# Optimization experiments

Measured on AMD Instinct MI355X. Metric: run time of the kernel, lower is better.

Reference implementation:

```python
import jax, jax.numpy as jnp
import numpy as np

B, S, D, H = 2, 2048, 1024, 16
HD = D // H  # head_dim = 64

def setup_inputs() -> dict:
    key = jax.random.key(0)
    ks = jax.random.split(key, 5)
    scale = 1.0 / np.sqrt(D)
    x = jax.random.normal(ks[0], (B, S, D), dtype=jnp.float32)
    Wq = jax.random.normal(ks[1], (D, D), dtype=jnp.float32) * scale
    Wk = jax.random.normal(ks[2], (D, D), dtype=jnp.float32) * scale
    Wv = jax.random.normal(ks[3], (D, D), dtype=jnp.float32) * scale
    Wf = jax.random.normal(ks[4], (D, D), dtype=jnp.float32) * scale
    z = jnp.zeros((D,), dtype=jnp.float32)
    return {"x": x, "Wq": Wq, "bq": z, "Wk": Wk, "bk": z, "Wv": Wv, "bv": z, "Wf": Wf, "bf": z}

def reference(x, Wq, bq, Wk, bk, Wv, bv, Wf, bf):
    # Linear layers follow torch convention: y = x @ W.T + b
    def split_heads(t):  # [B,S,D] -> [B,H,S,HD]
        return t.reshape(B, S, H, HD).transpose(0, 2, 1, 3)
    q = split_heads(x @ Wq.T + bq)
    k = split_heads(x @ Wk.T + bk)
    v = split_heads(x @ Wv.T + bv)
    scores = jnp.einsum('bhqd,bhkd->bhqk', q, k) / jnp.sqrt(jnp.float32(HD))
    causal = jnp.tril(jnp.ones((S, S), dtype=bool))  # [S,S]
    scores = jnp.where(causal[None, None], scores, -jnp.inf)
    attn = jax.nn.softmax(scores, axis=-1)
    out = jnp.einsum('bhqk,bhkd->bhqd', attn, v)
    out = out.transpose(0, 2, 1, 3).reshape(B, S, D)
    return out @ Wf.T + bf
```

## Files before the change

kernel.cpp:

```cpp
#include <hip/hip_runtime.h>
#include <stdint.h>

#define B_  2
#define S_  2048
#define D_  1024
#define H_  16
#define HD_ 64
#define M_  (B_*S_)

typedef __bf16 bf16x8 __attribute__((ext_vector_type(8)));
typedef float  f32x4  __attribute__((ext_vector_type(4)));

typedef const __attribute__((address_space(1))) void* gas_ptr;
typedef __attribute__((address_space(3))) void* las_ptr;

__device__ __forceinline__ uint16_t f32_to_bf16(float f) {
  uint32_t u = __float_as_uint(f);
  u += 0x7FFFu + ((u >> 16) & 1u);
  return (uint16_t)(u >> 16);
}

__device__ __forceinline__ void g2l16(const uint16_t* g, uint16_t* l) {
  __builtin_amdgcn_global_load_lds((gas_ptr)g, (las_ptr)l, 16, 0, 0);
}

__global__ void cast_all(const float* __restrict__ x,
                         const float* __restrict__ wq, const float* __restrict__ wk,
                         const float* __restrict__ wv, const float* __restrict__ wf,
                         uint16_t* __restrict__ xb,
                         uint16_t* __restrict__ wqb, uint16_t* __restrict__ wkb,
                         uint16_t* __restrict__ wvb, uint16_t* __restrict__ wfb) {
  const int X4 = M_ * D_ / 4;
  const int W4 = D_ * D_ / 4;
  int i = blockIdx.x * 256 + threadIdx.x;
  const float* src; uint16_t* dst; int off;
  if (i < X4) { src = x; dst = xb; off = i; }
  else {
    int j = i - X4;
    int w = j >> 18;
    off = j & (W4 - 1);
    src = (w == 0) ? wq : (w == 1) ? wk : (w == 2) ? wv : wf;
    dst = (w == 0) ? wqb : (w == 1) ? wkb : (w == 2) ? wvb : wfb;
  }
  float4 v = ((const float4*)src)[off];
  ushort4 o;
  o.x = f32_to_bf16(v.x); o.y = f32_to_bf16(v.y);
  o.z = f32_to_bf16(v.z); o.w = f32_to_bf16(v.w);
  ((ushort4*)dst)[off] = o;
}

__device__ __forceinline__ void gemm_tile_1024(
    const uint16_t* __restrict__ A, const uint16_t* __restrict__ B,
    int am0, int bn0, uint16_t* As, uint16_t* Bs, f32x4 (&acc)[4][4])
{
  const int tid  = threadIdx.x;
  const int wave = tid >> 6;
  const int lane = tid & 63;
  const int quad = lane >> 4;
  const int l16  = lane & 15;
  const int wm = (wave >> 1) * 64;
  const int wn = (wave & 1) * 64;

  #pragma unroll
  for (int i = 0; i < 4; ++i)
    #pragma unroll
    for (int j = 0; j < 4; ++j)
      #pragma unroll
      for (int e = 0; e < 4; ++e)
        acc[i][j][e] = 0.f;

  const int seg0 = wave * 64 + lane;
  const int seg1 = seg0 + 256;
  uint16_t* lA0 = As + (size_t)(wave * 64) * 8;
  uint16_t* lA1 = As + (size_t)(256 + wave * 64) * 8;
  uint16_t* lB0 = Bs + (size_t)(wave * 64) * 8;
  uint16_t* lB1 = Bs + (size_t)(256 + wave * 64) * 8;
  const uint16_t* gA0 = A + (size_t)(am0 + (seg0 >> 2)) * D_ + (seg0 & 3) * 8;
  const uint16_t* gA1 = A + (size_t)(am0 + (seg1 >> 2)) * D_ + (seg1 & 3) * 8;
  const uint16_t* gB0 = B + (size_t)(bn0 + (seg0 >> 2)) * D_ + (seg0 & 3) * 8;
  const uint16_t* gB1 = B + (size_t)(bn0 + (seg1 >> 2)) * D_ + (seg1 & 3) * 8;

  for (int k0 = 0; k0 < D_; k0 += 32) {
    g2l16(gA0 + k0, lA0);
    g2l16(gA1 + k0, lA1);
    g2l16(gB0 + k0, lB0);
    g2l16(gB1 + k0, lB1);
    __syncthreads();
    bf16x8 af[4], bfr[4];
    #pragma unroll
    for (int mt = 0; mt < 4; ++mt)
      af[mt] = *(const bf16x8*)(As + (wm + mt * 16 + l16) * 32 + quad * 8);
    #pragma unroll
    for (int nt = 0; nt < 4; ++nt)
      bfr[nt] = *(const bf16x8*)(Bs + (wn + nt * 16 + l16) * 32 + quad * 8);
    #pragma unroll
    for (int mt = 0; mt < 4; ++mt)
      #pragma unroll
      for (int nt = 0; nt < 4; ++nt)
        acc[mt][nt] = __builtin_amdgcn_mfma_f32_16x16x32_bf16(
            af[mt], bfr[nt], acc[mt][nt], 0, 0, 0);
    __syncthreads();
  }
}

__global__ __launch_bounds__(256)
void qkv_gemm(const uint16_t* __restrict__ xb,
              const uint16_t* __restrict__ wqb, const uint16_t* __restrict__ wkb,
              const uint16_t* __restrict__ wvb,
              const float* __restrict__ bqv, const float* __restrict__ bkv,
              const float* __restrict__ bvv,
              uint16_t* __restrict__ qout, uint16_t* __restrict__ kout,
              uint16_t* __restrict__ vtout)
{
  __shared__ __align__(16) uint16_t As[128 * 32];
  __shared__ __align__(16) uint16_t Bs[128 * 32];
  const int wsel = blockIdx.y >> 3;
  const int lane = threadIdx.x & 63, wave = threadIdx.x >> 6;
  const int quad = lane >> 4, l16 = lane & 15;
  const int wm = (wave >> 1) * 64, wn = (wave & 1) * 64;

  const uint16_t *Ap, *Bp;
  int m0e, n0e;
  if (wsel < 2) {
    Ap = xb; Bp = (wsel == 0) ? wqb : wkb;
    m0e = blockIdx.x * 128; n0e = (blockIdx.y & 7) * 128;
  } else {
    Ap = wvb; Bp = xb;
    m0e = (blockIdx.y & 7) * 128; n0e = blockIdx.x * 128;
  }
  f32x4 acc[4][4];
  gemm_tile_1024(Ap, Bp, m0e, n0e, As, Bs, acc);

  if (wsel < 2) {
    const float* bias = (wsel == 0) ? bqv : bkv;
    uint16_t* outp = (wsel == 0) ? qout : kout;
    const float scl = (wsel == 0) ? 0.18033688f : 1.0f;
    #pragma unroll
    for (int nt = 0; nt < 4; ++nt) {
      const int n = n0e + wn + nt * 16 + l16;
      const int h = n >> 6, hd = n & 63;
      const float bia = bias[n];
      #pragma unroll
      for (int mt = 0; mt < 4; ++mt) {
        #pragma unroll
        for (int r = 0; r < 4; ++r) {
          const int m = m0e + wm + mt * 16 + quad * 4 + r;
          const int bb = m >> 11, s = m & (S_ - 1);
          outp[(((size_t)(bb * H_ + h)) * S_ + s) * HD_ + hd] =
              f32_to_bf16((acc[mt][nt][r] + bia) * scl);
        }
      }
    }
  } else {
    #pragma unroll
    for (int mt = 0; mt < 4; ++mt) {
      #pragma unroll
      for (int r = 0; r < 4; ++r) {
        const int m = m0e + wm + mt * 16 + quad * 4 + r;
        const int h = m >> 6, hd = m & 63;
        const float bia = bvv[m];
        #pragma unroll
        for (int nt = 0; nt < 4; ++nt) {
          const int n = n0e + wn + nt * 16 + l16;
          const int bb = n >> 11, s = n & (S_ - 1);
          vtout[(((size_t)(bb * H_ + h)) * HD_ + hd) * S_ + s] =
              f32_to_bf16(acc[mt][nt][r] + bia);
        }
      }
    }
  }
}

__global__ __launch_bounds__(256)
void flash_attn(const uint16_t* __restrict__ qb, const uint16_t* __restrict__ kb,
                const uint16_t* __restrict__ vtb, uint16_t* __restrict__ ao)
{
  __shared__ __align__(16) uint16_t ks[2][64 * 32];
  __shared__ __align__(16) uint16_t vs[2][64 * 32];
  __shared__ __align__(16) uint16_t p_lds[4][16][72];

  const int bh = blockIdx.x;
  const int qt = (int)(gridDim.y - 1u - blockIdx.y);
  const int wave = threadIdx.x >> 6, lane = threadIdx.x & 63;
  const int quad = lane >> 4, l16 = lane & 15;
  const int q0 = qt * 64;

  const uint16_t* Q  = qb  + (size_t)bh * S_ * HD_;
  const uint16_t* Kp = kb  + (size_t)bh * S_ * HD_;
  const uint16_t* Vt = vtb + (size_t)bh * HD_ * S_;

  const int qrow = q0 + wave * 16;
  bf16x8 aq0 = *(const bf16x8*)(Q + (size_t)(qrow + l16) * HD_ + quad * 8);
  bf16x8 aq1 = *(const bf16x8*)(Q + (size_t)(qrow + l16) * HD_ + 32 + quad * 8);

  const uint16_t* sb[4]; uint16_t* sdst[4]; int sstep[4];
  #pragma unroll
  for (int j = 0; j < 4; ++j) {
    const int g = wave * 4 + j;
    if (g < 8) {
      const int c = (g >> 2) & 1, rb = g & 3;
      sdst[j] = &ks[c][rb * 512];
      sb[j] = Kp + (size_t)(rb * 16 + (lane >> 2)) * HD_ + c * 32 + (lane & 3) * 8;
      sstep[j] = 64 * HD_;
    } else {
      const int gg = g - 8, c = (gg >> 2) & 1, rb = gg & 3;
      sdst[j] = &vs[c][rb * 512];
      sb[j] = Vt + (size_t)(rb * 16 + (lane >> 2)) * S_ + c * 32 + (lane & 3) * 8;
      sstep[j] = 64;
    }
  }

  float lpart[4];
  f32x4 o[4];
  #pragma unroll
  for (int r = 0; r < 4; ++r) lpart[r] = 0.f;
  #pragma unroll
  for (int t = 0; t < 4; ++t)
    #pragma unroll
    for (int e = 0; e < 4; ++e) o[t][e] = 0.f;

  const int rowid = qrow + quad * 4;

  for (int kt = 0; kt <= qt; ++kt) {
    const int kbase = kt * 64;
    const bool diag = (kt == qt);

    #pragma unroll
    for (int j = 0; j < 4; ++j) {
      g2l16(sb[j], sdst[j]);
      sb[j] += sstep[j];
    }
    __syncthreads();

    bf16x8 kf0[4], kf1[4];
    #pragma unroll
    for (int nt = 0; nt < 4; ++nt) {
      kf0[nt] = *(const bf16x8*)(&ks[0][(nt * 16 + l16) * 32 + quad * 8]);
      kf1[nt] = *(const bf16x8*)(&ks[1][(nt * 16 + l16) * 32 + quad * 8]);
    }
    f32x4 sacc[4];
    #pragma unroll
    for (int nt = 0; nt < 4; ++nt) {
      #pragma unroll
      for (int e = 0; e < 4; ++e) sacc[nt][e] = 0.f;
      sacc[nt] = __builtin_amdgcn_mfma_f32_16x16x32_bf16(aq0, kf0[nt], sacc[nt], 0, 0, 0);
      sacc[nt] = __builtin_amdgcn_mfma_f32_16x16x32_bf16(aq1, kf1[nt], sacc[nt], 0, 0, 0);
    }

    bf16x8 vf0[4], vf1[4];
    #pragma unroll
    for (int t = 0; t < 4; ++t) {
      vf0[t] = *(const bf16x8*)(&vs[0][(t * 16 + l16) * 32 + quad * 8]);
      vf1[t] = *(const bf16x8*)(&vs[1][(t * 16 + l16) * 32 + quad * 8]);
    }

    #pragma unroll
    for (int nt = 0; nt < 4; ++nt) {
      const int kkc = kbase + nt * 16 + l16;
      #pragma unroll
      for (int r = 0; r < 4; ++r) {
        float p = __builtin_amdgcn_exp2f(sacc[nt][r]);
        if (diag && (kkc > rowid + r)) p = 0.f;
        lpart[r] += p;
        p_lds[wave][quad * 4 + r][nt * 16 + l16] = f32_to_bf16(p);
      }
    }

    bf16x8 ap0 = *(const bf16x8*)(&p_lds[wave][l16][quad * 8]);
    bf16x8 ap1 = *(const bf16x8*)(&p_lds[wave][l16][32 + quad * 8]);
    #pragma unroll
    for (int t = 0; t < 4; ++t) {
      o[t] = __builtin_amdgcn_mfma_f32_16x16x32_bf16(ap0, vf0[t], o[t], 0, 0, 0);
      o[t] = __builtin_amdgcn_mfma_f32_16x16x32_bf16(ap1, vf1[t], o[t], 0, 0, 0);
    }
    __syncthreads();
  }

  #pragma unroll
  for (int r = 0; r < 4; ++r) {
    lpart[r] += __shfl_xor(lpart[r], 1, 64);
    lpart[r] += __shfl_xor(lpart[r], 2, 64);
    lpart[r] += __shfl_xor(lpart[r], 4, 64);
    lpart[r] += __shfl_xor(lpart[r], 8, 64);
  }
  const int bb = bh >> 4, h = bh & 15;
  #pragma unroll
  for (int t = 0; t < 4; ++t) {
    #pragma unroll
    for (int r = 0; r < 4; ++r) {
      const float ov = o[t][r] / lpart[r];
      ao[((size_t)(bb * S_ + rowid + r)) * D_ + h * HD_ + t * 16 + l16] =
          f32_to_bf16(ov);
    }
  }
}

__global__ __launch_bounds__(256)
void out_gemm(const uint16_t* __restrict__ ab, const uint16_t* __restrict__ wfb,
              const float* __restrict__ bfv, float* __restrict__ out)
{
  __shared__ __align__(16) uint16_t As[64 * 32];
  __shared__ __align__(16) uint16_t Bs[128 * 32];
  const int m0 = blockIdx.x * 64;
  const int n0 = blockIdx.y * 128;
  const int lane = threadIdx.x & 63, wave = threadIdx.x >> 6;
  const int quad = lane >> 4, l16 = lane & 15;
  const int wm = (wave >> 1) * 32, wn = (wave & 1) * 64;

  f32x4 acc[2][4];
  #pragma unroll
  for (int i = 0; i < 2; ++i)
    #pragma unroll
    for (int j = 0; j < 4; ++j)
      #pragma unroll
      for (int e = 0; e < 4; ++e)
        acc[i][j][e] = 0.f;

  const int segA = wave * 64 + lane;
  const int segB0 = segA, segB1 = segA + 256;
  uint16_t* lA  = As + (size_t)(wave * 64) * 8;
  uint16_t* lB0 = Bs + (size_t)(wave * 64) * 8;
  uint16_t* lB1 = Bs + (size_t)(256 + wave * 64) * 8;
  const uint16_t* gA  = ab  + (size_t)(m0 + (segA  >> 2)) * D_ + (segA  & 3) * 8;
  const uint16_t* gB0 = wfb + (size_t)(n0 + (segB0 >> 2)) * D_ + (segB0 & 3) * 8;
  const uint16_t* gB1 = wfb + (size_t)(n0 + (segB1 >> 2)) * D_ + (segB1 & 3) * 8;

  for (int k0 = 0; k0 < D_; k0 += 32) {
    g2l16(gA  + k0, lA);
    g2l16(gB0 + k0, lB0);
    g2l16(gB1 + k0, lB1);
    __syncthreads();
    bf16x8 af[2], bfr[4];
    #pragma unroll
    for (int mt = 0; mt < 2; ++mt)
      af[mt] = *(const bf16x8*)(As + (wm + mt * 16 + l16) * 32 + quad * 8);
    #pragma unroll
    for (int nt = 0; nt < 4; ++nt)
      bfr[nt] = *(const bf16x8*)(Bs + (wn + nt * 16 + l16) * 32 + quad * 8);
    #pragma unroll
    for (int mt = 0; mt < 2; ++mt)
      #pragma unroll
      for (int nt = 0; nt < 4; ++nt)
        acc[mt][nt] = __builtin_amdgcn_mfma_f32_16x16x32_bf16(
            af[mt], bfr[nt], acc[mt][nt], 0, 0, 0);
    __syncthreads();
  }

  #pragma unroll
  for (int nt = 0; nt < 4; ++nt) {
    const int n = n0 + wn + nt * 16 + l16;
    const float bia = bfv[n];
    #pragma unroll
    for (int mt = 0; mt < 2; ++mt) {
      #pragma unroll
      for (int r = 0; r < 4; ++r) {
        const int m = m0 + wm + mt * 16 + quad * 4 + r;
        out[(size_t)m * D_ + n] = acc[mt][nt][r] + bia;
      }
    }
  }
}

extern "C" void kernel_launch(void* const* d_in, const int* in_sizes, int n_in,
                              void* d_out, int out_size, void* d_ws, size_t ws_size,
                              hipStream_t stream) {
  (void)in_sizes; (void)n_in; (void)out_size; (void)ws_size;
  const float* x  = (const float*)d_in[0];
  const float* Wq = (const float*)d_in[1];
  const float* bq = (const float*)d_in[2];
  const float* Wk = (const float*)d_in[3];
  const float* bk = (const float*)d_in[4];
  const float* Wv = (const float*)d_in[5];
  const float* bv = (const float*)d_in[6];
  const float* Wf = (const float*)d_in[7];
  const float* bf = (const float*)d_in[8];
  float* out = (float*)d_out;

  uint16_t* ws = (uint16_t*)d_ws;
  uint16_t* xb   = ws;
  uint16_t* wqb  = xb  + (size_t)M_ * D_;
  uint16_t* wkb  = wqb + (size_t)D_ * D_;
  uint16_t* wvb  = wkb + (size_t)D_ * D_;
  uint16_t* wfb  = wvb + (size_t)D_ * D_;
  uint16_t* qbuf = wfb + (size_t)D_ * D_;
  uint16_t* kbuf = qbuf + (size_t)M_ * D_;
  uint16_t* vtb  = kbuf + (size_t)M_ * D_;
  uint16_t* aob  = vtb  + (size_t)M_ * D_;

  const int CAST_BLOCKS = (M_ * D_ / 4 + 4 * (D_ * D_ / 4)) / 256;
  cast_all<<<CAST_BLOCKS, 256, 0, stream>>>(x, Wq, Wk, Wv, Wf,
                                            xb, wqb, wkb, wvb, wfb);

  qkv_gemm<<<dim3(32, 24), 256, 0, stream>>>(xb, wqb, wkb, wvb, bq, bk, bv,
                                             qbuf, kbuf, vtb);
  flash_attn<<<dim3(32, 32), 256, 0, stream>>>(qbuf, kbuf, vtb, aob);
  out_gemm<<<dim3(64, 8), 256, 0, stream>>>(aob, wfb, bf, out);
}
```

Before: 198.3 us.

## Swizzle LDS tile layout and shrink QKV GEMM tile to 64x128

Applies an XOR swizzle to the 16-byte chunks staged into LDS via global_load_lds (permuting source addresses) and matches it in the fragment reads for the GEMMs and the flash-attention K/V tiles, to reduce LDS bank conflicts. The QKV GEMM tile shrinks from 128x128 to 64x128, doubling the grid to give more blocks and better occupancy, and out_gemm now reuses the shared tile routine. Smaller tiles mean more redundant global loads per FLOP.

```diff
diff --git a/kernel.cpp b/kernel.cpp
--- a/kernel.cpp
+++ b/kernel.cpp
@@ -22,6 +22,10 @@
 
 __device__ __forceinline__ void g2l16(const uint16_t* g, uint16_t* l) {
   __builtin_amdgcn_global_load_lds((gas_ptr)g, (las_ptr)l, 16, 0, 0);
+}
+
+__device__ __forceinline__ int swz_src(int s) {
+  return (s >> 2) * D_ + (((s & 3) ^ ((s >> 3) & 3)) * 8);
 }
 
 __global__ void cast_all(const float* __restrict__ x,
@@ -49,52 +53,50 @@
   ((ushort4*)dst)[off] = o;
 }
 
-__device__ __forceinline__ void gemm_tile_1024(
+__device__ __forceinline__ void gemm_tile_64x128(
     const uint16_t* __restrict__ A, const uint16_t* __restrict__ B,
-    int am0, int bn0, uint16_t* As, uint16_t* Bs, f32x4 (&acc)[4][4])
+    int am0, int bn0, uint16_t* As, uint16_t* Bs, f32x4 (&acc)[2][4])
 {
   const int tid  = threadIdx.x;
   const int wave = tid >> 6;
   const int lane = tid & 63;
   const int quad = lane >> 4;
   const int l16  = lane & 15;
-  const int wm = (wave >> 1) * 64;
+  const int wm = (wave >> 1) * 32;
   const int wn = (wave & 1) * 64;
-
-  #pragma unroll
-  for (int i = 0; i < 4; ++i)
+  const int sw = quad ^ ((l16 >> 1) & 3);
+
+  #pragma unroll
+  for (int i = 0; i < 2; ++i)
     #pragma unroll
     for (int j = 0; j < 4; ++j)
       #pragma unroll
       for (int e = 0; e < 4; ++e)
         acc[i][j][e] = 0.f;
 
-  const int seg0 = wave * 64 + lane;
-  const int seg1 = seg0 + 256;
-  uint16_t* lA0 = As + (size_t)(wave * 64) * 8;
-  uint16_t* lA1 = As + (size_t)(256 + wave * 64) * 8;
+  const int sA  = wave * 64 + lane;
+  const int sB1 = sA + 256;
+  uint16_t* lA  = As + (size_t)(wave * 64) * 8;
   uint16_t* lB0 = Bs + (size_t)(wave * 64) * 8;
   uint16_t* lB1 = Bs + (size_t)(256 + wave * 64) * 8;
-  const uint16_t* gA0 = A + (size_t)(am0 + (seg0 >> 2)) * D_ + (seg0 & 3) * 8;
-  const uint16_t* gA1 = A + (size_t)(am0 + (seg1 >> 2)) * D_ + (seg1 & 3) * 8;
-  const uint16_t* gB0 = B + (size_t)(bn0 + (seg0 >> 2)) * D_ + (seg0 & 3) * 8;
-  const uint16_t* gB1 = B + (size_t)(bn0 + (seg1 >> 2)) * D_ + (seg1 & 3) * 8;
+  const uint16_t* gA  = A + (size_t)am0 * D_ + swz_src(sA);
+  const uint16_t* gB0 = B + (size_t)bn0 * D_ + swz_src(sA);
+  const uint16_t* gB1 = B + (size_t)bn0 * D_ + swz_src(sB1);
 
   for (int k0 = 0; k0 < D_; k0 += 32) {
-    g2l16(gA0 + k0, lA0);
-    g2l16(gA1 + k0, lA1);
+    g2l16(gA  + k0, lA);
     g2l16(gB0 + k0, lB0);
     g2l16(gB1 + k0, lB1);
     __syncthreads();
-    bf16x8 af[4], bfr[4];
-    #pragma unroll
-    for (int mt = 0; mt < 4; ++mt)
-      af[mt] = *(const bf16x8*)(As + (wm + mt * 16 + l16) * 32 + quad * 8);
+    bf16x8 af[2], bfr[4];
+    #pragma unroll
+    for (int mt = 0; mt < 2; ++mt)
+      af[mt] = *(const bf16x8*)(As + ((wm + mt * 16 + l16) * 4 + sw) * 8);
     #pragma unroll
     for (int nt = 0; nt < 4; ++nt)
-      bfr[nt] = *(const bf16x8*)(Bs + (wn + nt * 16 + l16) * 32 + quad * 8);
-    #pragma unroll
-    for (int mt = 0; mt < 4; ++mt)
+      bfr[nt] = *(const bf16x8*)(Bs + ((wn + nt * 16 + l16) * 4 + sw) * 8);
+    #pragma unroll
+    for (int mt = 0; mt < 2; ++mt)
       #pragma unroll
       for (int nt = 0; nt < 4; ++nt)
         acc[mt][nt] = __builtin_amdgcn_mfma_f32_16x16x32_bf16(
@@ -112,24 +114,25 @@
               uint16_t* __restrict__ qout, uint16_t* __restrict__ kout,
               uint16_t* __restrict__ vtout)
 {
-  __shared__ __align__(16) uint16_t As[128 * 32];
+  __shared__ __align__(16) uint16_t As[64 * 32];
   __shared__ __align__(16) uint16_t Bs[128 * 32];
   const int wsel = blockIdx.y >> 3;
   const int lane = threadIdx.x & 63, wave = threadIdx.x >> 6;
   const int quad = lane >> 4, l16 = lane & 15;
-  const int wm = (wave >> 1) * 64, wn = (wave & 1) * 64;
+  const int wm = (wave >> 1) * 32, wn = (wave & 1) * 64;
 
   const uint16_t *Ap, *Bp;
   int m0e, n0e;
   if (wsel < 2) {
     Ap = xb; Bp = (wsel == 0) ? wqb : wkb;
-    m0e = blockIdx.x * 128; n0e = (blockIdx.y & 7) * 128;
+    m0e = blockIdx.x * 64; n0e = (blockIdx.y & 7) * 128;
   } else {
+    const int vi = (blockIdx.y & 7) * 64 + blockIdx.x;
     Ap = wvb; Bp = xb;
-    m0e = (blockIdx.y & 7) * 128; n0e = blockIdx.x * 128;
-  }
-  f32x4 acc[4][4];
-  gemm_tile_1024(Ap, Bp, m0e, n0e, As, Bs, acc);
+    m0e = (vi & 15) * 64; n0e = (vi >> 4) * 128;
+  }
+  f32x4 acc[2][4];
+  gemm_tile_64x128(Ap, Bp, m0e, n0e, As, Bs, acc);
 
   if (wsel < 2) {
     const float* bias = (wsel == 0) ? bqv : bkv;
@@ -141,7 +144,7 @@
       const int h = n >> 6, hd = n & 63;
       const float bia = bias[n];
       #pragma unroll
-      for (int mt = 0; mt < 4; ++mt) {
+      for (int mt = 0; mt < 2; ++mt) {
         #pragma unroll
         for (int r = 0; r < 4; ++r) {
           const int m = m0e + wm + mt * 16 + quad * 4 + r;
@@ -153,7 +156,7 @@
     }
   } else {
     #pragma unroll
-    for (int mt = 0; mt < 4; ++mt) {
+    for (int mt = 0; mt < 2; ++mt) {
       #pragma unroll
       for (int r = 0; r < 4; ++r) {
         const int m = m0e + wm + mt * 16 + quad * 4 + r;
@@ -183,6 +186,7 @@
   const int qt = (int)(gridDim.y - 1u - blockIdx.y);
   const int wave = threadIdx.x >> 6, lane = threadIdx.x & 63;
   const int quad = lane >> 4, l16 = lane & 15;
+  const int sw = quad ^ ((l16 >> 1) & 3);
   const int q0 = qt * 64;
 
   const uint16_t* Q  = qb  + (size_t)bh * S_ * HD_;
@@ -193,6 +197,8 @@
   bf16x8 aq0 = *(const bf16x8*)(Q + (size_t)(qrow + l16) * HD_ + quad * 8);
   bf16x8 aq1 = *(const bf16x8*)(Q + (size_t)(qrow + l16) * HD_ + 32 + quad * 8);
 
+  const int srow = lane >> 2;
+  const int schk = (lane & 3) ^ ((lane >> 3) & 3);
   const uint16_t* sb[4]; uint16_t* sdst[4]; int sstep[4];
   #pragma unroll
   for (int j = 0; j < 4; ++j) {
@@ -200,12 +206,12 @@
     if (g < 8) {
       const int c = (g >> 2) & 1, rb = g & 3;
       sdst[j] = &ks[c][rb * 512];
-      sb[j] = Kp + (size_t)(rb * 16 + (lane >> 2)) * HD_ + c * 32 + (lane & 3) * 8;
+      sb[j] = Kp + (size_t)(rb * 16 + srow) * HD_ + c * 32 + schk * 8;
       sstep[j] = 64 * HD_;
     } else {
       const int gg = g - 8, c = (gg >> 2) & 1, rb = gg & 3;
       sdst[j] = &vs[c][rb * 512];
-      sb[j] = Vt + (size_t)(rb * 16 + (lane >> 2)) * S_ + c * 32 + (lane & 3) * 8;
+      sb[j] = Vt + (size_t)(rb * 16 + srow) * S_ + c * 32 + schk * 8;
       sstep[j] = 64;
     }
   }
@@ -235,8 +241,8 @@
     bf16x8 kf0[4], kf1[4];
     #pragma unroll
     for (int nt = 0; nt < 4; ++nt) {
-      kf0[nt] = *(const bf16x8*)(&ks[0][(nt * 16 + l16) * 32 + quad * 8]);
-      kf1[nt] = *(const bf16x8*)(&ks[1][(nt * 16 + l16) * 32 + quad * 8]);
+      kf0[nt] = *(const bf16x8*)(&ks[0][((nt * 16 + l16) * 4 + sw) * 8]);
+      kf1[nt] = *(const bf16x8*)(&ks[1][((nt * 16 + l16) * 4 + sw) * 8]);
     }
     f32x4 sacc[4];
     #pragma unroll
@@ -250,8 +256,8 @@
     bf16x8 vf0[4], vf1[4];
     #pragma unroll
     for (int t = 0; t < 4; ++t) {
-      vf0[t] = *(const bf16x8*)(&vs[0][(t * 16 + l16) * 32 + quad * 8]);
-      vf1[t] = *(const bf16x8*)(&vs[1][(t * 16 + l16) * 32 + quad * 8]);
+      vf0[t] = *(const bf16x8*)(&vs[0][((t * 16 + l16) * 4 + sw) * 8]);
+      vf1[t] = *(const bf16x8*)(&vs[1][((t * 16 + l16) * 4 + sw) * 8]);
     }
 
     #pragma unroll
@@ -303,49 +309,11 @@
   __shared__ __align__(16) uint16_t Bs[128 * 32];
   const int m0 = blockIdx.x * 64;
   const int n0 = blockIdx.y * 128;
+  f32x4 acc[2][4];
+  gemm_tile_64x128(ab, wfb, m0, n0, As, Bs, acc);
   const int lane = threadIdx.x & 63, wave = threadIdx.x >> 6;
   const int quad = lane >> 4, l16 = lane & 15;
   const int wm = (wave >> 1) * 32, wn = (wave & 1) * 64;
-
-  f32x4 acc[2][4];
-  #pragma unroll
-  for (int i = 0; i < 2; ++i)
-    #pragma unroll
-    for (int j = 0; j < 4; ++j)
-      #pragma unroll
-      for (int e = 0; e < 4; ++e)
-        acc[i][j][e] = 0.f;
-
-  const int segA = wave * 64 + lane;
-  const int segB0 = segA, segB1 = segA + 256;
-  uint16_t* lA  = As + (size_t)(wave * 64) * 8;
-  uint16_t* lB0 = Bs + (size_t)(wave * 64) * 8;
-  uint16_t* lB1 = Bs + (size_t)(256 + wave * 64) * 8;
-  const uint16_t* gA  = ab  + (size_t)(m0 + (segA  >> 2)) * D_ + (segA  & 3) * 8;
-  const uint16_t* gB0 = wfb + (size_t)(n0 + (segB0 >> 2)) * D_ + (segB0 & 3) * 8;
-  const uint16_t* gB1 = wfb + (size_t)(n0 + (segB1 >> 2)) * D_ + (segB1 & 3) * 8;
-
-  for (int k0 = 0; k0 < D_; k0 += 32) {
-    g2l16(gA  + k0, lA);
-    g2l16(gB0 + k0, lB0);
-    g2l16(gB1 + k0, lB1);
-    __syncthreads();
-    bf16x8 af[2], bfr[4];
-    #pragma unroll
-    for (int mt = 0; mt < 2; ++mt)
-      af[mt] = *(const bf16x8*)(As + (wm + mt * 16 + l16) * 32 + quad * 8);
-    #pragma unroll
-    for (int nt = 0; nt < 4; ++nt)
-      bfr[nt] = *(const bf16x8*)(Bs + (wn + nt * 16 + l16) * 32 + quad * 8);
-    #pragma unroll
-    for (int mt = 0; mt < 2; ++mt)
-      #pragma unroll
-      for (int nt = 0; nt < 4; ++nt)
-        acc[mt][nt] = __builtin_amdgcn_mfma_f32_16x16x32_bf16(
-            af[mt], bfr[nt], acc[mt][nt], 0, 0, 0);
-    __syncthreads();
-  }
-
   #pragma unroll
   for (int nt = 0; nt < 4; ++nt) {
     const int n = n0 + wn + nt * 16 + l16;
@@ -391,7 +359,7 @@
   cast_all<<<CAST_BLOCKS, 256, 0, stream>>>(x, Wq, Wk, Wv, Wf,
                                             xb, wqb, wkb, wvb, wfb);
 
-  qkv_gemm<<<dim3(32, 24), 256, 0, stream>>>(xb, wqb, wkb, wvb, bq, bk, bv,
+  qkv_gemm<<<dim3(64, 24), 256, 0, stream>>>(xb, wqb, wkb, wvb, bq, bk, bv,
                                              qbuf, kbuf, vtb);
   flash_attn<<<dim3(32, 32), 256, 0, stream>>>(qbuf, kbuf, vtb, aob);
   out_gemm<<<dim3(64, 8), 256, 0, stream>>>(aob, wfb, bf, out);
```

Result: faster. 194.1 us (-2.2%).

## XOR-swizzle LDS tiles to avoid bank conflicts and reorder GEMM grid

Applied to the files above, without the earlier changes.

Applies an XOR swizzle to the 16-byte chunk index when loading A/B tiles and K/V tiles into LDS: global source addresses are permuted so the direct global-to-LDS writes land swizzled, and the MFMA fragment reads use the matching swizzle. The aim is to remove LDS bank conflicts on the row-strided bf16x8 reads in all three GEMM and attention kernels. It also transposes the GEMM launch grids so consecutive blocks share the same activation rows and walk across weight tiles, which is meant to improve L2 reuse. The extra index arithmetic is small, and correctness depends on the load permutation and read swizzle matching exactly.

```diff
diff --git a/kernel.cpp b/kernel.cpp
--- a/kernel.cpp
+++ b/kernel.cpp
@@ -22,6 +22,10 @@
 
 __device__ __forceinline__ void g2l16(const uint16_t* g, uint16_t* l) {
   __builtin_amdgcn_global_load_lds((gas_ptr)g, (las_ptr)l, 16, 0, 0);
+}
+
+__device__ __forceinline__ int swz_src(int s) {
+  return (s >> 2) * D_ + (((s & 3) ^ ((s >> 3) & 3)) * 8);
 }
 
 __global__ void cast_all(const float* __restrict__ x,
@@ -49,7 +53,7 @@
   ((ushort4*)dst)[off] = o;
 }
 
-__device__ __forceinline__ void gemm_tile_1024(
+__device__ __forceinline__ void gemm_tile_128_swz(
     const uint16_t* __restrict__ A, const uint16_t* __restrict__ B,
     int am0, int bn0, uint16_t* As, uint16_t* Bs, f32x4 (&acc)[4][4])
 {
@@ -60,6 +64,7 @@
   const int l16  = lane & 15;
   const int wm = (wave >> 1) * 64;
   const int wn = (wave & 1) * 64;
+  const int sw = quad ^ ((l16 >> 1) & 3);
 
   #pragma unroll
   for (int i = 0; i < 4; ++i)
@@ -69,16 +74,16 @@
       for (int e = 0; e < 4; ++e)
         acc[i][j][e] = 0.f;
 
-  const int seg0 = wave * 64 + lane;
-  const int seg1 = seg0 + 256;
+  const int s0 = wave * 64 + lane;
+  const int s1 = s0 + 256;
   uint16_t* lA0 = As + (size_t)(wave * 64) * 8;
   uint16_t* lA1 = As + (size_t)(256 + wave * 64) * 8;
   uint16_t* lB0 = Bs + (size_t)(wave * 64) * 8;
   uint16_t* lB1 = Bs + (size_t)(256 + wave * 64) * 8;
-  const uint16_t* gA0 = A + (size_t)(am0 + (seg0 >> 2)) * D_ + (seg0 & 3) * 8;
-  const uint16_t* gA1 = A + (size_t)(am0 + (seg1 >> 2)) * D_ + (seg1 & 3) * 8;
-  const uint16_t* gB0 = B + (size_t)(bn0 + (seg0 >> 2)) * D_ + (seg0 & 3) * 8;
-  const uint16_t* gB1 = B + (size_t)(bn0 + (seg1 >> 2)) * D_ + (seg1 & 3) * 8;
+  const uint16_t* gA0 = A + (size_t)am0 * D_ + swz_src(s0);
+  const uint16_t* gA1 = A + (size_t)am0 * D_ + swz_src(s1);
+  const uint16_t* gB0 = B + (size_t)bn0 * D_ + swz_src(s0);
+  const uint16_t* gB1 = B + (size_t)bn0 * D_ + swz_src(s1);
 
   for (int k0 = 0; k0 < D_; k0 += 32) {
     g2l16(gA0 + k0, lA0);
@@ -89,10 +94,10 @@
     bf16x8 af[4], bfr[4];
     #pragma unroll
     for (int mt = 0; mt < 4; ++mt)
-      af[mt] = *(const bf16x8*)(As + (wm + mt * 16 + l16) * 32 + quad * 8);
+      af[mt] = *(const bf16x8*)(As + ((wm + mt * 16 + l16) * 4 + sw) * 8);
     #pragma unroll
     for (int nt = 0; nt < 4; ++nt)
-      bfr[nt] = *(const bf16x8*)(Bs + (wn + nt * 16 + l16) * 32 + quad * 8);
+      bfr[nt] = *(const bf16x8*)(Bs + ((wn + nt * 16 + l16) * 4 + sw) * 8);
     #pragma unroll
     for (int mt = 0; mt < 4; ++mt)
       #pragma unroll
@@ -114,7 +119,9 @@
 {
   __shared__ __align__(16) uint16_t As[128 * 32];
   __shared__ __align__(16) uint16_t Bs[128 * 32];
-  const int wsel = blockIdx.y >> 3;
+  const int wsel = blockIdx.x >> 3;
+  const int nsel = blockIdx.x & 7;
+  const int mtile = blockIdx.y;
   const int lane = threadIdx.x & 63, wave = threadIdx.x >> 6;
   const int quad = lane >> 4, l16 = lane & 15;
   const int wm = (wave >> 1) * 64, wn = (wave & 1) * 64;
@@ -123,13 +130,13 @@
   int m0e, n0e;
   if (wsel < 2) {
     Ap = xb; Bp = (wsel == 0) ? wqb : wkb;
-    m0e = blockIdx.x * 128; n0e = (blockIdx.y & 7) * 128;
+    m0e = mtile * 128; n0e = nsel * 128;
   } else {
     Ap = wvb; Bp = xb;
-    m0e = (blockIdx.y & 7) * 128; n0e = blockIdx.x * 128;
+    m0e = nsel * 128; n0e = mtile * 128;
   }
   f32x4 acc[4][4];
-  gemm_tile_1024(Ap, Bp, m0e, n0e, As, Bs, acc);
+  gemm_tile_128_swz(Ap, Bp, m0e, n0e, As, Bs, acc);
 
   if (wsel < 2) {
     const float* bias = (wsel == 0) ? bqv : bkv;
@@ -183,6 +190,7 @@
   const int qt = (int)(gridDim.y - 1u - blockIdx.y);
   const int wave = threadIdx.x >> 6, lane = threadIdx.x & 63;
   const int quad = lane >> 4, l16 = lane & 15;
+  const int sw = quad ^ ((l16 >> 1) & 3);
   const int q0 = qt * 64;
 
   const uint16_t* Q  = qb  + (size_t)bh * S_ * HD_;
@@ -193,6 +201,8 @@
   bf16x8 aq0 = *(const bf16x8*)(Q + (size_t)(qrow + l16) * HD_ + quad * 8);
   bf16x8 aq1 = *(const bf16x8*)(Q + (size_t)(qrow + l16) * HD_ + 32 + quad * 8);
 
+  const int srow = lane >> 2;
+  const int schk = (lane & 3) ^ ((lane >> 3) & 3);
   const uint16_t* sb[4]; uint16_t* sdst[4]; int sstep[4];
   #pragma unroll
   for (int j = 0; j < 4; ++j) {
@@ -200,12 +210,12 @@
     if (g < 8) {
       const int c = (g >> 2) & 1, rb = g & 3;
       sdst[j] = &ks[c][rb * 512];
-      sb[j] = Kp + (size_t)(rb * 16 + (lane >> 2)) * HD_ + c * 32 + (lane & 3) * 8;
+      sb[j] = Kp + (size_t)(rb * 16 + srow) * HD_ + c * 32 + schk * 8;
       sstep[j] = 64 * HD_;
     } else {
       const int gg = g - 8, c = (gg >> 2) & 1, rb = gg & 3;
       sdst[j] = &vs[c][rb * 512];
-      sb[j] = Vt + (size_t)(rb * 16 + (lane >> 2)) * S_ + c * 32 + (lane & 3) * 8;
+      sb[j] = Vt + (size_t)(rb * 16 + srow) * S_ + c * 32 + schk * 8;
       sstep[j] = 64;
     }
   }
@@ -235,8 +245,8 @@
     bf16x8 kf0[4], kf1[4];
     #pragma unroll
     for (int nt = 0; nt < 4; ++nt) {
-      kf0[nt] = *(const bf16x8*)(&ks[0][(nt * 16 + l16) * 32 + quad * 8]);
-      kf1[nt] = *(const bf16x8*)(&ks[1][(nt * 16 + l16) * 32 + quad * 8]);
+      kf0[nt] = *(const bf16x8*)(&ks[0][((nt * 16 + l16) * 4 + sw) * 8]);
+      kf1[nt] = *(const bf16x8*)(&ks[1][((nt * 16 + l16) * 4 + sw) * 8]);
     }
     f32x4 sacc[4];
     #pragma unroll
@@ -250,8 +260,8 @@
     bf16x8 vf0[4], vf1[4];
     #pragma unroll
     for (int t = 0; t < 4; ++t) {
-      vf0[t] = *(const bf16x8*)(&vs[0][(t * 16 + l16) * 32 + quad * 8]);
-      vf1[t] = *(const bf16x8*)(&vs[1][(t * 16 + l16) * 32 + quad * 8]);
+      vf0[t] = *(const bf16x8*)(&vs[0][((t * 16 + l16) * 4 + sw) * 8]);
+      vf1[t] = *(const bf16x8*)(&vs[1][((t * 16 + l16) * 4 + sw) * 8]);
     }
 
     #pragma unroll
@@ -301,11 +311,12 @@
 {
   __shared__ __align__(16) uint16_t As[64 * 32];
   __shared__ __align__(16) uint16_t Bs[128 * 32];
-  const int m0 = blockIdx.x * 64;
-  const int n0 = blockIdx.y * 128;
+  const int m0 = blockIdx.y * 64;
+  const int n0 = blockIdx.x * 128;
   const int lane = threadIdx.x & 63, wave = threadIdx.x >> 6;
   const int quad = lane >> 4, l16 = lane & 15;
   const int wm = (wave >> 1) * 32, wn = (wave & 1) * 64;
+  const int sw = quad ^ ((l16 >> 1) & 3);
 
   f32x4 acc[2][4];
   #pragma unroll
@@ -316,14 +327,14 @@
       for (int e = 0; e < 4; ++e)
         acc[i][j][e] = 0.f;
 
-  const int segA = wave * 64 + lane;
-  const int segB0 = segA, segB1 = segA + 256;
+  const int sA  = wave * 64 + lane;
+  const int sB1 = sA + 256;
   uint16_t* lA  = As + (size_t)(wave * 64) * 8;
   uint16_t* lB0 = Bs + (size_t)(wave * 64) * 8;
   uint16_t* lB1 = Bs + (size_t)(256 + wave * 64) * 8;
-  const uint16_t* gA  = ab  + (size_t)(m0 + (segA  >> 2)) * D_ + (segA  & 3) * 8;
-  const uint16_t* gB0 = wfb + (size_t)(n0 + (segB0 >> 2)) * D_ + (segB0 & 3) * 8;
-  const uint16_t* gB1 = wfb + (size_t)(n0 + (segB1 >> 2)) * D_ + (segB1 & 3) * 8;
+  const uint16_t* gA  = ab  + (size_t)m0 * D_ + swz_src(sA);
+  const uint16_t* gB0 = wfb + (size_t)n0 * D_ + swz_src(sA);
+  const uint16_t* gB1 = wfb + (size_t)n0 * D_ + swz_src(sB1);
 
   for (int k0 = 0; k0 < D_; k0 += 32) {
     g2l16(gA  + k0, lA);
@@ -333,10 +344,10 @@
     bf16x8 af[2], bfr[4];
     #pragma unroll
     for (int mt = 0; mt < 2; ++mt)
-      af[mt] = *(const bf16x8*)(As + (wm + mt * 16 + l16) * 32 + quad * 8);
+      af[mt] = *(const bf16x8*)(As + ((wm + mt * 16 + l16) * 4 + sw) * 8);
     #pragma unroll
     for (int nt = 0; nt < 4; ++nt)
-      bfr[nt] = *(const bf16x8*)(Bs + (wn + nt * 16 + l16) * 32 + quad * 8);
+      bfr[nt] = *(const bf16x8*)(Bs + ((wn + nt * 16 + l16) * 4 + sw) * 8);
     #pragma unroll
     for (int mt = 0; mt < 2; ++mt)
       #pragma unroll
@@ -391,8 +402,8 @@
   cast_all<<<CAST_BLOCKS, 256, 0, stream>>>(x, Wq, Wk, Wv, Wf,
                                             xb, wqb, wkb, wvb, wfb);
 
-  qkv_gemm<<<dim3(32, 24), 256, 0, stream>>>(xb, wqb, wkb, wvb, bq, bk, bv,
+  qkv_gemm<<<dim3(24, 32), 256, 0, stream>>>(xb, wqb, wkb, wvb, bq, bk, bv,
                                              qbuf, kbuf, vtb);
   flash_attn<<<dim3(32, 32), 256, 0, stream>>>(qbuf, kbuf, vtb, aob);
-  out_gemm<<<dim3(64, 8), 256, 0, stream>>>(aob, wfb, bf, out);
-}
+  out_gemm<<<dim3(8, 64), 256, 0, stream>>>(aob, wfb, bf, out);
+}
```

Measured after the change: 190.5 us. -3.9%, faster.
